# Optimization experiments

Measured on AMD Instinct MI355X. Metric: run time of the kernel, lower is better.

The kernel has to match this reference:

```python
import jax, jax.numpy as jnp
import numpy as np

EPS = 1e-06


def _create_circular_masks(h, w):
    # Faithful to the torch code: y spans width, x spans height -> mask shape (w, h).
    # Only used with square feature maps (h == w), matching the module's implicit assumption.
    cen_w, cen_h = w // 2, h // 2
    y = np.arange(-cen_w, w - cen_w).reshape(-1, 1)
    x = np.arange(-cen_h, h - cen_h).reshape(1, -1)
    y2, x2 = y * y, x * x
    r2 = x2 + y2
    masks = [r2 <= 0]
    max_r = int(np.sqrt(r2.max())) + 1
    quadrants = [(1, 1), (-1, 1), (1, -1), (-1, -1)]  # (sign_x, sign_y)
    for radius in range(1, max_r):
        lo, hi = (radius - 1) ** 2, radius ** 2
        for sx, sy in quadrants:
            quad = (sx * x >= 0) & (sy * y >= 0)
            masks.append((r2 > lo) & (r2 <= hi) & quad)  # ring mask
            masks.append((r2 <= hi) & quad)              # circle mask
    return np.stack(masks).astype(np.float32)  # [M, w, h] == [M, h, w] for square maps


def _l2_normalize(v):
    # v: [B, C]; torch norms over dim=1 with eps added to the norm
    return v / (jnp.linalg.norm(v, axis=1, keepdims=True) + EPS)


def setup_inputs() -> dict:
    key = jax.random.key(0)
    x = jax.random.normal(key, (32, 1024, 28, 28), dtype=jnp.float32)
    return {"x": x}


def reference(x) -> jnp.ndarray:
    B, C, H, W = x.shape
    masks = jnp.asarray(_create_circular_masks(H, W))  # [M, H, W] static constant
    # Global descriptor: max-pool over full map, then channel-wise L2 normalize.
    v = _l2_normalize(jnp.max(x, axis=(2, 3)))  # [B, C]
    # Accumulate masked-max descriptors; scan over the (fixed) mask set keeps
    # peak memory at one masked feature map instead of M of them.
    def step(acc, mask):
        vt = jnp.max(x * mask, axis=(2, 3))  # masked max-pool (zeros included, as in torch)
        return acc + _l2_normalize(vt), None
    v, _ = jax.lax.scan(step, v, masks)
    return v[:, :, None, None]  # [B, C, 1, 1] to match F.max_pool2d output shape
```

## Files before the change

### kernel.cpp

```cpp
#include <hip/hip_runtime.h>
#include <math.h>

#define B_DIM 32
#define C_DIM 1024
#define HW 28
#define MAP 784
#define NMASK 153
#define NTERM 154
#define NROW 160
#define NBIN 77
#define DUMMY_BIN 77
#define MAX1 28
#define MAX2 6

struct Sched {
    unsigned short off1[MAX1][64];
    unsigned short off2[MAX2][64];
    unsigned char  binA[64];
    unsigned char  binB[64];
    bool ok;
};

constexpr Sched build_sched() {
    Sched S{};
    S.ok = true;
    short px[NBIN][40] = {};
    int   n[NBIN] = {};
    for (int i = 0; i < 28; ++i)
        for (int j = 0; j < 28; ++j) {
            int dy = i - 14, dx = j - 14, r2 = dx * dx + dy * dy;
            int p = i * 28 + j;
            if (r2 == 0) { px[0][n[0]++] = (short)p; continue; }
            if (r2 > 361) continue;
            int r = 0; while (r * r < r2) ++r;
            const int sx[4] = {1, -1, 1, -1}, sy[4] = {1, 1, -1, -1};
            for (int q = 0; q < 4; ++q)
                if (sx[q] * dx >= 0 && sy[q] * dy >= 0) {
                    int b = 1 + q * 19 + (r - 1);
                    if (n[b] >= 40) { S.ok = false; continue; }
                    px[b][n[b]++] = (short)p;
                }
        }
    int ord[NBIN] = {};
    for (int k = 0; k < NBIN; ++k) ord[k] = k;
    for (int a = 0; a < NBIN; ++a) {
        int best = a;
        for (int c = a + 1; c < NBIN; ++c)
            if (n[ord[c]] > n[ord[best]]) best = c;
        int t = ord[a]; ord[a] = ord[best]; ord[best] = t;
    }
    for (int l = 0; l < 64; ++l) {
        S.binA[l] = (unsigned char)ord[l];
        S.binB[l] = (l >= 51) ? (unsigned char)ord[64 + (l - 51)]
                              : (unsigned char)DUMMY_BIN;
        if (n[ord[l]] > MAX1) S.ok = false;
        if (l >= 51 && n[ord[64 + (l - 51)]] > MAX2) S.ok = false;
    }
    {
        bool used[64][40] = {};
        for (int s = 0; s < MAX1; ++s) {
            int bankcnt[32] = {};
            for (int l = 0; l < 64; ++l) {
                int bin = S.binA[l], cnt = n[bin];
                int bestp = 0, bestload = 1 << 30; bool haveUnused = false;
                for (int t = 0; t < cnt; ++t)
                    if (!used[l][t]) {
                        int load = bankcnt[px[bin][t] % 32];
                        if (!haveUnused || load < bestload) { haveUnused = true; bestload = load; bestp = t; }
                    }
                if (!haveUnused)
                    for (int t = 0; t < cnt; ++t) {
                        int load = bankcnt[px[bin][t] % 32];
                        if (load < bestload) { bestload = load; bestp = t; }
                    }
                int p = px[bin][bestp];
                if (haveUnused) used[l][bestp] = true;
                S.off1[s][l] = (unsigned short)(p * 4);
                bankcnt[p % 32]++;
            }
        }
        for (int l = 0; l < 64; ++l)
            for (int t = 0; t < n[S.binA[l]]; ++t)
                if (!used[l][t]) S.ok = false;
    }
    {
        bool used[64][40] = {};
        for (int s = 0; s < MAX2; ++s) {
            int bankcnt[32] = {};
            for (int l = 0; l < 64; ++l) {
                if (S.binB[l] == DUMMY_BIN) {
                    S.off2[s][l] = (unsigned short)((l % 32) * 4);
                    continue;
                }
                int bin = S.binB[l], cnt = n[bin];
                int bestp = 0, bestload = 1 << 30; bool haveUnused = false;
                for (int t = 0; t < cnt; ++t)
                    if (!used[l][t]) {
                        int load = bankcnt[px[bin][t] % 32];
                        if (!haveUnused || load < bestload) { haveUnused = true; bestload = load; bestp = t; }
                    }
                if (!haveUnused)
                    for (int t = 0; t < cnt; ++t) {
                        int load = bankcnt[px[bin][t] % 32];
                        if (load < bestload) { bestload = load; bestp = t; }
                    }
                int p = px[bin][bestp];
                if (haveUnused) used[l][bestp] = true;
                S.off2[s][l] = (unsigned short)(p * 4);
                bankcnt[p % 32]++;
            }
        }
        for (int l = 0; l < 64; ++l)
            if (S.binB[l] != DUMMY_BIN)
                for (int t = 0; t < n[S.binB[l]]; ++t)
                    if (!used[l][t]) S.ok = false;
    }
    return S;
}

static_assert(build_sched().ok, "schedule overflow / unplaced pixel");
__constant__ Sched d_sched = build_sched();

__global__ __launch_bounds__(256) void cac_stageA(const float* __restrict__ x,
                                                  float* __restrict__ vt,
                                                  float* __restrict__ partial) {
    __shared__ __align__(16) float smap[4][MAP];
    __shared__ float sbin[4][NBIN + 1];
    __shared__ float spref[4][4][20];
    __shared__ float ssq[4][NROW];

    const int wave = threadIdx.x >> 6;
    const int lane = threadIdx.x & 63;
    const int pair = blockIdx.x * 4 + wave;

    const float4* xp4 = (const float4*)(x + (size_t)pair * MAP);
    float4* sm4 = (float4*)smap[wave];
    float gmax = -INFINITY;
    #pragma unroll
    for (int it = 0; it < 3; ++it) {
        float4 v = xp4[it * 64 + lane];
        sm4[it * 64 + lane] = v;
        gmax = fmaxf(fmaxf(gmax, fmaxf(v.x, v.y)), fmaxf(v.z, v.w));
    }
    if (lane < 4) {
        float4 v = xp4[192 + lane];
        sm4[192 + lane] = v;
        gmax = fmaxf(fmaxf(gmax, fmaxf(v.x, v.y)), fmaxf(v.z, v.w));
    }
    __syncthreads();

    const char* base = (const char*)smap[wave];
    float m1 = 0.0f, m2 = 0.0f;
    #pragma unroll
    for (int s = 0; s < MAX1; ++s)
        m1 = fmaxf(m1, *(const float*)(base + d_sched.off1[s][lane]));
    #pragma unroll
    for (int s = 0; s < MAX2; ++s)
        m2 = fmaxf(m2, *(const float*)(base + d_sched.off2[s][lane]));

    sbin[wave][d_sched.binA[lane]] = m1;
    sbin[wave][d_sched.binB[lane]] = m2;

    #pragma unroll
    for (int off = 32; off; off >>= 1)
        gmax = fmaxf(gmax, __shfl_xor(gmax, off, 64));
    __syncthreads();

    if (lane < 4) {
        float run = sbin[wave][0];
        #pragma unroll
        for (int r = 1; r < 20; ++r) {
            run = fmaxf(run, sbin[wave][1 + lane * 19 + (r - 1)]);
            spref[wave][lane][r] = run;
        }
    }
    __syncthreads();

    float* rowp = vt + (size_t)pair * NROW;
    #pragma unroll
    for (int i = 0; i < 3; ++i) {
        int k = lane + i * 64;
        if (k < NROW) {
            float val;
            if (k == 0) val = sbin[wave][0];
            else if (k == NMASK) val = gmax;
            else if (k < NMASK) {
                int t = k - 1, r = (t >> 3) + 1, q = (t >> 1) & 3;
                val = (t & 1) ? spref[wave][q][r]
                              : sbin[wave][1 + q * 19 + (r - 1)];
            } else val = 0.0f;
            rowp[k] = val;
            ssq[wave][k] = val * val;
        }
    }
    __syncthreads();

    if (threadIdx.x < NROW) {
        int t = threadIdx.x;
        partial[(size_t)blockIdx.x * NROW + t] =
            ssq[0][t] + ssq[1][t] + ssq[2][t] + ssq[3][t];
    }
}

__global__ __launch_bounds__(192) void cac_stageB(const float* __restrict__ partial,
                                                  float* __restrict__ invn) {
    const int b = blockIdx.x, t = threadIdx.x;
    if (t >= NROW) return;
    const float* p = partial + (size_t)b * 256 * NROW + t;
    float s = 0.0f;
    #pragma unroll 8
    for (int r = 0; r < 256; ++r) s += p[(size_t)r * NROW];
    invn[b * NROW + t] = (t < NTERM) ? 1.0f / (sqrtf(s) + 1e-6f) : 0.0f;
}

__global__ __launch_bounds__(128) void cac_stageC(const float* __restrict__ vt,
                                                  const float* __restrict__ invn,
                                                  float* __restrict__ out) {
    __shared__ __align__(16) float sinv[NROW];
    const int pair = blockIdx.x * 128 + threadIdx.x;
    const int b = pair >> 10;
    for (int i = threadIdx.x; i < NROW; i += 128)
        sinv[i] = invn[b * NROW + i];
    __syncthreads();
    const float4* row = (const float4*)(vt + (size_t)pair * NROW);
    const float4* w4 = (const float4*)sinv;
    float acc = 0.0f;
    #pragma unroll
    for (int i = 0; i < NROW / 4; ++i) {
        float4 v = row[i], w = w4[i];
        acc += v.x * w.x + v.y * w.y + v.z * w.z + v.w * w.w;
    }
    out[pair] = acc;
}

extern "C" void kernel_launch(void* const* d_in, const int* in_sizes, int n_in,
                              void* d_out, int out_size, void* d_ws, size_t ws_size,
                              hipStream_t stream) {
    const float* x = (const float*)d_in[0];
    float* out = (float*)d_out;

    float* vt      = (float*)d_ws;
    float* partial = vt + (size_t)B_DIM * C_DIM * NROW;
    float* invn    = partial + (size_t)8192 * NROW;

    cac_stageA<<<(B_DIM * C_DIM) / 4, 256, 0, stream>>>(x, vt, partial);
    cac_stageB<<<B_DIM, 192, 0, stream>>>(partial, invn);
    cac_stageC<<<(B_DIM * C_DIM) / 128, 128, 0, stream>>>(vt, invn, out);
}
```

Baseline: 167.7 us.

## Process eight maps per wave with prefetch, fold norm reduction into final kernel

Each wave now handles eight (batch, channel) maps in a loop, prefetching the next map's global data into registers while the current one is reduced. Block-wide syncs are replaced by wave barriers, and the serial prefix max is replaced by a shuffle-based scan. The separate norm-reduction kernel is merged into the final dot-product kernel, cutting one launch. The workspace row grows to 192 floats so each lane writes three aligned elements, at the cost of more intermediate traffic and fewer blocks in flight.

```diff
diff --git a/kernel.cpp b/kernel.cpp
--- a/kernel.cpp
+++ b/kernel.cpp
@@ -3,15 +3,15 @@
 
 #define B_DIM 32
 #define C_DIM 1024
-#define HW 28
 #define MAP 784
 #define NMASK 153
 #define NTERM 154
-#define NROW 160
+#define NROW 192
 #define NBIN 77
 #define DUMMY_BIN 77
 #define MAX1 28
 #define MAX2 6
+#define MPW 8
 
 struct Sched {
     unsigned short off1[MAX1][64];
@@ -121,116 +121,145 @@
 static_assert(build_sched().ok, "schedule overflow / unplaced pixel");
 __constant__ Sched d_sched = build_sched();
 
-__global__ __launch_bounds__(256) void cac_stageA(const float* __restrict__ x,
-                                                  float* __restrict__ vt,
-                                                  float* __restrict__ partial) {
+__device__ __forceinline__ int term_addr(int k) {
+    if (k == 0) return 0;
+    if (k >= NMASK) return DUMMY_BIN;
+    int t = k - 1, q = (t >> 1) & 3, rm1 = t >> 3;
+    return (t & 1) ? 78 + q * 19 + rm1
+                   : 1 + q * 19 + rm1;
+}
+
+__global__ __launch_bounds__(256) void cac_k1(const float* __restrict__ x,
+                                              float* __restrict__ vt,
+                                              float* __restrict__ partial) {
     __shared__ __align__(16) float smap[4][MAP];
-    __shared__ float sbin[4][NBIN + 1];
-    __shared__ float spref[4][4][20];
-    __shared__ float ssq[4][NROW];
+    __shared__ float sbuf[4][160];
+    __shared__ float ssqred[4][NROW];
 
     const int wave = threadIdx.x >> 6;
     const int lane = threadIdx.x & 63;
-    const int pair = blockIdx.x * 4 + wave;
-
-    const float4* xp4 = (const float4*)(x + (size_t)pair * MAP);
-    float4* sm4 = (float4*)smap[wave];
-    float gmax = -INFINITY;
+    const int pair0 = blockIdx.x * 32 + wave * MPW;
+
+    const int linA = lane % 19;
+    const bool inA = lane < 57, inB = lane < 19;
+    const int rbA = 1 + lane;
+    const int rbB = inB ? 58 + lane : DUMMY_BIN;
+    const int a0 = term_addr(lane);
+    const int a1 = term_addr(lane + 64);
+    const int a2 = term_addr(lane + 128);
+
+    const float4 NEG4 = make_float4(-INFINITY, -INFINITY, -INFINITY, -INFINITY);
+    const float4* xp4 = (const float4*)(x + (size_t)pair0 * MAP);
+    float4 t0 = xp4[lane], t1 = xp4[64 + lane], t2 = xp4[128 + lane];
+    float4 t3 = NEG4;
+    if (lane < 4) t3 = xp4[192 + lane];
+
+    float* smw = smap[wave];
+    float* sbw = sbuf[wave];
+    float sq0 = 0.0f, sq1 = 0.0f, sq2 = 0.0f;
+
     #pragma unroll
-    for (int it = 0; it < 3; ++it) {
-        float4 v = xp4[it * 64 + lane];
-        sm4[it * 64 + lane] = v;
-        gmax = fmaxf(fmaxf(gmax, fmaxf(v.x, v.y)), fmaxf(v.z, v.w));
-    }
-    if (lane < 4) {
-        float4 v = xp4[192 + lane];
-        sm4[192 + lane] = v;
-        gmax = fmaxf(fmaxf(gmax, fmaxf(v.x, v.y)), fmaxf(v.z, v.w));
-    }
+    for (int m = 0; m < MPW; ++m) {
+        ((float4*)smw)[lane]       = t0;
+        ((float4*)smw)[64 + lane]  = t1;
+        ((float4*)smw)[128 + lane] = t2;
+        if (lane < 4) ((float4*)smw)[192 + lane] = t3;
+        float gmax = fmaxf(fmaxf(fmaxf(t0.x, t0.y), fmaxf(t0.z, t0.w)),
+                           fmaxf(fmaxf(t1.x, t1.y), fmaxf(t1.z, t1.w)));
+        gmax = fmaxf(gmax, fmaxf(fmaxf(t2.x, t2.y), fmaxf(t2.z, t2.w)));
+        gmax = fmaxf(gmax, fmaxf(fmaxf(t3.x, t3.y), fmaxf(t3.z, t3.w)));
+
+        if (m < MPW - 1) {
+            const float4* np4 = (const float4*)(x + (size_t)(pair0 + m + 1) * MAP);
+            t0 = np4[lane]; t1 = np4[64 + lane]; t2 = np4[128 + lane];
+            t3 = NEG4;
+            if (lane < 4) t3 = np4[192 + lane];
+        }
+        __builtin_amdgcn_wave_barrier();
+
+        const char* base = (const char*)smw;
+        float m1 = 0.0f, m2v = 0.0f;
+        #pragma unroll
+        for (int s = 0; s < MAX1; ++s)
+            m1 = fmaxf(m1, *(const float*)(base + d_sched.off1[s][lane]));
+        #pragma unroll
+        for (int s = 0; s < MAX2; ++s)
+            m2v = fmaxf(m2v, *(const float*)(base + d_sched.off2[s][lane]));
+        sbw[d_sched.binA[lane]] = m1;
+        sbw[d_sched.binB[lane]] = m2v;
+
+        #pragma unroll
+        for (int off = 32; off; off >>= 1)
+            gmax = fmaxf(gmax, __shfl_xor(gmax, off, 64));
+        __builtin_amdgcn_wave_barrier();
+
+        float cval = sbw[0];
+        float rA = fmaxf(sbw[rbA], cval);
+        float rB = fmaxf(sbw[rbB], cval);
+        #pragma unroll
+        for (int s = 1; s <= 16; s <<= 1) {
+            float uA = __shfl_up(rA, s, 64);
+            float uB = __shfl_up(rB, s, 64);
+            if (linA >= s) rA = fmaxf(rA, uA);
+            if (lane >= s) rB = fmaxf(rB, uB);
+        }
+        if (inA) sbw[78 + lane] = rA;
+        if (inB) sbw[135 + lane] = rB;
+        __builtin_amdgcn_wave_barrier();
+
+        float r0 = sbw[a0];
+        float r1 = sbw[a1];
+        float r2 = sbw[a2];
+        r2 = (lane == 25) ? gmax : (lane < 26 ? r2 : 0.0f);
+
+        float* rowp = vt + (size_t)(pair0 + m) * NROW;
+        rowp[lane]       = r0;
+        rowp[64 + lane]  = r1;
+        rowp[128 + lane] = r2;
+        sq0 += r0 * r0; sq1 += r1 * r1; sq2 += r2 * r2;
+        __builtin_amdgcn_wave_barrier();
+    }
+
+    ssqred[wave][lane]       = sq0;
+    ssqred[wave][lane + 64]  = sq1;
+    ssqred[wave][lane + 128] = sq2;
     __syncthreads();
-
-    const char* base = (const char*)smap[wave];
-    float m1 = 0.0f, m2 = 0.0f;
-    #pragma unroll
-    for (int s = 0; s < MAX1; ++s)
-        m1 = fmaxf(m1, *(const float*)(base + d_sched.off1[s][lane]));
-    #pragma unroll
-    for (int s = 0; s < MAX2; ++s)
-        m2 = fmaxf(m2, *(const float*)(base + d_sched.off2[s][lane]));
-
-    sbin[wave][d_sched.binA[lane]] = m1;
-    sbin[wave][d_sched.binB[lane]] = m2;
-
-    #pragma unroll
-    for (int off = 32; off; off >>= 1)
-        gmax = fmaxf(gmax, __shfl_xor(gmax, off, 64));
-    __syncthreads();
-
-    if (lane < 4) {
-        float run = sbin[wave][0];
-        #pragma unroll
-        for (int r = 1; r < 20; ++r) {
-            run = fmaxf(run, sbin[wave][1 + lane * 19 + (r - 1)]);
-            spref[wave][lane][r] = run;
-        }
-    }
-    __syncthreads();
-
-    float* rowp = vt + (size_t)pair * NROW;
-    #pragma unroll
-    for (int i = 0; i < 3; ++i) {
-        int k = lane + i * 64;
-        if (k < NROW) {
-            float val;
-            if (k == 0) val = sbin[wave][0];
-            else if (k == NMASK) val = gmax;
-            else if (k < NMASK) {
-                int t = k - 1, r = (t >> 3) + 1, q = (t >> 1) & 3;
-                val = (t & 1) ? spref[wave][q][r]
-                              : sbin[wave][1 + q * 19 + (r - 1)];
-            } else val = 0.0f;
-            rowp[k] = val;
-            ssq[wave][k] = val * val;
-        }
-    }
-    __syncthreads();
-
     if (threadIdx.x < NROW) {
         int t = threadIdx.x;
         partial[(size_t)blockIdx.x * NROW + t] =
-            ssq[0][t] + ssq[1][t] + ssq[2][t] + ssq[3][t];
-    }
-}
-
-__global__ __launch_bounds__(192) void cac_stageB(const float* __restrict__ partial,
-                                                  float* __restrict__ invn) {
-    const int b = blockIdx.x, t = threadIdx.x;
-    if (t >= NROW) return;
-    const float* p = partial + (size_t)b * 256 * NROW + t;
-    float s = 0.0f;
-    #pragma unroll 8
-    for (int r = 0; r < 256; ++r) s += p[(size_t)r * NROW];
-    invn[b * NROW + t] = (t < NTERM) ? 1.0f / (sqrtf(s) + 1e-6f) : 0.0f;
-}
-
-__global__ __launch_bounds__(128) void cac_stageC(const float* __restrict__ vt,
-                                                  const float* __restrict__ invn,
-                                                  float* __restrict__ out) {
+            ssqred[0][t] + ssqred[1][t] + ssqred[2][t] + ssqred[3][t];
+    }
+}
+
+__global__ __launch_bounds__(256) void cac_k2(const float* __restrict__ vt,
+                                              const float* __restrict__ partial,
+                                              float* __restrict__ out) {
     __shared__ __align__(16) float sinv[NROW];
-    const int pair = blockIdx.x * 128 + threadIdx.x;
-    const int b = pair >> 10;
-    for (int i = threadIdx.x; i < NROW; i += 128)
-        sinv[i] = invn[b * NROW + i];
+    const int b = blockIdx.x >> 3;
+
+    if (threadIdx.x < NROW) {
+        int t = threadIdx.x;
+        const float* p = partial + (size_t)(b * 32) * NROW + t;
+        float s = 0.0f;
+        #pragma unroll
+        for (int j = 0; j < 32; ++j) s += p[j * NROW];
+        sinv[t] = (t < NTERM) ? 1.0f / (sqrtf(s) + 1e-6f) : 0.0f;
+    }
     __syncthreads();
-    const float4* row = (const float4*)(vt + (size_t)pair * NROW);
-    const float4* w4 = (const float4*)sinv;
+
+    const int local = threadIdx.x >> 1;
+    const int half  = threadIdx.x & 1;
+    const int pair  = blockIdx.x * 128 + local;
+    const float4* row = (const float4*)(vt + (size_t)pair * NROW + half * 96);
+    const float4* w4  = (const float4*)sinv + half * 24;
     float acc = 0.0f;
     #pragma unroll
-    for (int i = 0; i < NROW / 4; ++i) {
+    for (int i = 0; i < 24; ++i) {
         float4 v = row[i], w = w4[i];
         acc += v.x * w.x + v.y * w.y + v.z * w.z + v.w * w.w;
     }
-    out[pair] = acc;
+    acc += __shfl_xor(acc, 1, 64);
+    if (!half) out[pair] = acc;
 }
 
 extern "C" void kernel_launch(void* const* d_in, const int* in_sizes, int n_in,
@@ -241,9 +270,7 @@
 
     float* vt      = (float*)d_ws;
     float* partial = vt + (size_t)B_DIM * C_DIM * NROW;
-    float* invn    = partial + (size_t)8192 * NROW;
-
-    cac_stageA<<<(B_DIM * C_DIM) / 4, 256, 0, stream>>>(x, vt, partial);
-    cac_stageB<<<B_DIM, 192, 0, stream>>>(partial, invn);
-    cac_stageC<<<(B_DIM * C_DIM) / 128, 128, 0, stream>>>(vt, invn, out);
-}
+
+    cac_k1<<<1024, 256, 0, stream>>>(x, vt, partial);
+    cac_k2<<<256, 256, 0, stream>>>(vt, partial, out);
+}
```

Result: faster. 162.2 us (-3.3%).
